# Optimization experiments

Measured on AMD Instinct MI355X. Metric: run time of the kernel, lower is better.

The kernel has to match this reference:

```python
import jax, jax.numpy as jnp
import numpy as np

N_NODES = 100000
N_EDGES = 3200000
D_FEAT = 128
N_LAYERS = 2

def setup_inputs() -> dict:
    key = jax.random.key(0)
    k1, k2, k3, k4 = jax.random.split(key, 4)
    x = jax.random.normal(k1, (N_NODES, D_FEAT), dtype=jnp.float32)
    edge_row = jax.random.randint(k2, (N_EDGES,), 0, N_NODES)  # destination (spmm output row)
    edge_col = jax.random.randint(k3, (N_EDGES,), 0, N_NODES)  # source node
    edge_vals = jax.random.uniform(k4, (N_EDGES,), dtype=jnp.float32)
    scalars = jnp.ones((N_LAYERS,), dtype=jnp.float32)  # per-layer learned scalar (init ones)
    return {"x": x, "edge_row": edge_row, "edge_col": edge_col,
            "edge_vals": edge_vals, "scalars": scalars}

def reference(x, edge_row, edge_col, edge_vals, scalars):
    # ScalarSGC forward with dropout p=0 (identity). Same adjacency each layer.
    for l in range(N_LAYERS):
        h = scalars[l] * x                      # scalar * x
        msg = edge_vals[:, None] * h[edge_col]  # [E, D] gather + scale
        agg = jax.ops.segment_sum(msg, edge_row, num_segments=N_NODES)  # spmm
        x = jax.nn.elu(agg)
    return x
```

## Files before the change

kernel.cpp:

```cpp
#include <hip/hip_runtime.h>
#include <math.h>
#include <stdint.h>


#define D_FEAT 128
#define D2     64
#define SCAN_TILE 1024

#define PB 256
#define PT 1024
#define RB_BITS 9
#define ROWS_PER_BUCKET 512
#define COL_BITS 17
#define CACHE_CAP 17152

__device__ __forceinline__ uint32_t f2bf(float f) {
    uint32_t u = __float_as_uint(f);
    return (u + 0x7FFFu + ((u >> 16) & 1u)) >> 16;
}
__device__ __forceinline__ float bf_lo(uint32_t w) { return __uint_as_float(w << 16); }
__device__ __forceinline__ float bf_hi(uint32_t w) { return __uint_as_float(w & 0xFFFF0000u); }

__global__ void convert_kernel(const float2* __restrict__ xin, uint32_t* __restrict__ xbf, int n2) {
    int i = blockIdx.x * blockDim.x + threadIdx.x;
    if (i < n2) {
        float2 f = xin[i];
        xbf[i] = f2bf(f.x) | (f2bf(f.y) << 16);
    }
}

__global__ __launch_bounds__(PT) void coarse_count_kernel(const int* __restrict__ row,
                                                          int* __restrict__ cnt,
                                                          int E, int nbuck) {
    __shared__ int hist[256];
    const int t = threadIdx.x;
    if (t < 256) hist[t] = 0;
    __syncthreads();
    const int stride = PB * PT;
    for (int i = blockIdx.x * PT + t; i < E; i += stride)
        atomicAdd(&hist[row[i] >> RB_BITS], 1);
    __syncthreads();
    if (t < nbuck) cnt[t * PB + blockIdx.x] = hist[t];
}

__global__ __launch_bounds__(SCAN_TILE) void scan1_kernel(const int* __restrict__ counts,
                                                          int* __restrict__ excl,
                                                          int* __restrict__ tileSums, int n) {
    __shared__ int wsum[16];
    const int tid  = threadIdx.x;
    const int lane = tid & 63;
    const int wave = tid >> 6;
    const int i    = blockIdx.x * SCAN_TILE + tid;

    int v = (i < n) ? counts[i] : 0;
    int incl = v;
    #pragma unroll
    for (int off = 1; off < 64; off <<= 1) {
        int t = __shfl_up(incl, off, 64);
        if (lane >= off) incl += t;
    }
    if (lane == 63) wsum[wave] = incl;
    __syncthreads();
    if (wave == 0) {
        int s = (lane < 16) ? wsum[lane] : 0;
        #pragma unroll
        for (int off = 1; off < 16; off <<= 1) {
            int t = __shfl_up(s, off, 64);
            if (lane >= off) s += t;
        }
        if (lane < 16) wsum[lane] = s;
    }
    __syncthreads();
    int wbase = (wave == 0) ? 0 : wsum[wave - 1];
    if (i < n) excl[i] = wbase + (incl - v);
    if (tid == 0) tileSums[blockIdx.x] = wsum[15];
}

__global__ __launch_bounds__(1024) void scan2_kernel(const int* __restrict__ tileSums,
                                                     int* __restrict__ tileBase,
                                                     int* __restrict__ total_out, int nb) {
    __shared__ int buf[1024];
    const int tid = threadIdx.x;
    int v = (tid < nb) ? tileSums[tid] : 0;
    buf[tid] = v;
    __syncthreads();
    #pragma unroll
    for (int off = 1; off < 1024; off <<= 1) {
        int t = (tid >= off) ? buf[tid - off] : 0;
        __syncthreads();
        buf[tid] += t;
        __syncthreads();
    }
    if (tid < nb) tileBase[tid] = buf[tid] - v;
    if (tid == nb - 1) *total_out = buf[tid];
}

__global__ __launch_bounds__(PT) void partition_kernel(const int* __restrict__ row,
                                                       const int* __restrict__ col,
                                                       const float* __restrict__ val,
                                                       const int* __restrict__ cnt,
                                                       const int* __restrict__ tileBase,
                                                       int2* __restrict__ pack2,
                                                       int E, int nbuck) {
    __shared__ int cur[256];
    const int t = threadIdx.x;
    if (t < nbuck) {
        int idx = t * PB + blockIdx.x;
        cur[t] = cnt[idx] + tileBase[idx >> 10];
    }
    __syncthreads();
    const int stride = PB * PT;
    for (int i = blockIdx.x * PT + t; i < E; i += stride) {
        int r = row[i];
        int pos = atomicAdd(&cur[r >> RB_BITS], 1);
        pack2[pos] = make_int2(col[i] | ((r & (ROWS_PER_BUCKET - 1)) << COL_BITS),
                               __float_as_int(val[i]));
    }
}

__global__ __launch_bounds__(1024) void fine_sort_kernel(const int* __restrict__ cnt,
                                                         const int* __restrict__ tileBase,
                                                         const int2* __restrict__ pack2,
                                                         int2* __restrict__ pack,
                                                         int* __restrict__ offsets,
                                                         int E, int N, int nbuck) {
    extern __shared__ int2 ecache[];
    __shared__ int buf[1024];
    __shared__ int cur[ROWS_PER_BUCKET];
    const int b = blockIdx.x;
    const int t = threadIdx.x;
    const int start = cnt[b << 8] + tileBase[b >> 2];
    const int end   = (b == nbuck - 1) ? E : (cnt[(b + 1) << 8] + tileBase[(b + 1) >> 2]);
    const int n  = end - start;
    const int nc = (n < CACHE_CAP) ? n : CACHE_CAP;

    for (int i = t; i < nc; i += 1024) ecache[i] = pack2[start + i];
    buf[t] = 0;
    __syncthreads();

    for (int i = t; i < n; i += 1024) {
        int key = (i < nc) ? ecache[i].x : pack2[start + i].x;
        atomicAdd(&buf[((unsigned)key) >> COL_BITS], 1);
    }
    __syncthreads();

    int v = buf[t];
    for (int off = 1; off < 1024; off <<= 1) {
        int tv = (t >= off) ? buf[t - off] : 0;
        __syncthreads();
        buf[t] += tv;
        __syncthreads();
    }
    int excl = buf[t] - v;
    if (t < ROWS_PER_BUCKET) {
        int r = (b << RB_BITS) + t;
        if (r < N) offsets[r] = start + excl;
        cur[t] = excl;
    }
    if (b == 0 && t == 0) offsets[N] = E;
    __syncthreads();

    for (int i = t; i < n; i += 1024) {
        int2 w = (i < nc) ? ecache[i] : pack2[start + i];
        int lr = ((unsigned)w.x) >> COL_BITS;
        int p = atomicAdd(&cur[lr], 1);
        pack[start + p] = make_int2(w.x & ((1 << COL_BITS) - 1), w.y);
    }
}

template <int OUT_BF16>
__global__ __launch_bounds__(256) void spmm_elu_kernel(
    const int* __restrict__ offsets, const int2* __restrict__ pack,
    const uint32_t* __restrict__ xin, void* __restrict__ xout,
    const float* __restrict__ scalars, int layer, int N) {
    const int wave = threadIdx.x >> 6;
    const uint32_t lane = threadIdx.x & 63;
    const int r    = blockIdx.x * 4 + wave;
    if (r >= N) return;

    int e = offsets[r];
    const int end = offsets[r + 1];

    float a0x = 0.f, a0y = 0.f, a1x = 0.f, a1y = 0.f;
    float a2x = 0.f, a2y = 0.f, a3x = 0.f, a3y = 0.f;

    for (; e + 4 <= end; e += 4) {
        int2 p0 = pack[e], p1 = pack[e + 1], p2 = pack[e + 2], p3 = pack[e + 3];
        uint32_t w0 = xin[(((uint32_t)p0.x) << 6) + lane];
        uint32_t w1 = xin[(((uint32_t)p1.x) << 6) + lane];
        uint32_t w2 = xin[(((uint32_t)p2.x) << 6) + lane];
        uint32_t w3 = xin[(((uint32_t)p3.x) << 6) + lane];
        float v0 = __int_as_float(p0.y), v1 = __int_as_float(p1.y);
        float v2 = __int_as_float(p2.y), v3 = __int_as_float(p3.y);
        a0x += v0 * bf_lo(w0); a0y += v0 * bf_hi(w0);
        a1x += v1 * bf_lo(w1); a1y += v1 * bf_hi(w1);
        a2x += v2 * bf_lo(w2); a2y += v2 * bf_hi(w2);
        a3x += v3 * bf_lo(w3); a3y += v3 * bf_hi(w3);
    }
    for (; e < end; ++e) {
        int2 p = pack[e];
        uint32_t w = xin[(((uint32_t)p.x) << 6) + lane];
        float v = __int_as_float(p.y);
        a0x += v * bf_lo(w); a0y += v * bf_hi(w);
    }

    float ax = (a0x + a1x) + (a2x + a3x);
    float ay = (a0y + a1y) + (a2y + a3y);
    const float s = scalars[layer];
    ax *= s; ay *= s;
    ax = (ax > 0.f) ? ax : (expf(ax) - 1.f);
    ay = (ay > 0.f) ? ay : (expf(ay) - 1.f);

    if (OUT_BF16) {
        ((uint32_t*)xout)[(size_t)r * D2 + lane] = f2bf(ax) | (f2bf(ay) << 16);
    } else {
        ((float2*)xout)[(size_t)r * D2 + lane] = make_float2(ax, ay);
    }
}

extern "C" void kernel_launch(void* const* d_in, const int* in_sizes, int n_in,
                              void* d_out, int out_size, void* d_ws, size_t ws_size,
                              hipStream_t stream) {
    const float* x         = (const float*)d_in[0];
    const int*   edge_row  = (const int*)d_in[1];
    const int*   edge_col  = (const int*)d_in[2];
    const float* edge_vals = (const float*)d_in[3];
    const float* scalars   = (const float*)d_in[4];

    const int N = in_sizes[0] / D_FEAT;
    const int E = in_sizes[1];
    const int nbuck = (N + ROWS_PER_BUCKET - 1) >> RB_BITS;
    const int M = nbuck * PB;
    const int NB = (M + SCAN_TILE - 1) / SCAN_TILE;

    char*  ws  = (char*)d_ws;
    size_t off = 0;
    auto alloc = [&](size_t bytes) -> void* {
        off = (off + 255) & ~(size_t)255;
        void* p = ws + off;
        off += bytes;
        return p;
    };
    int*      offsets  = (int*)alloc((size_t)(N + 1) * sizeof(int));
    int*      cnt      = (int*)alloc((size_t)(M + 1) * sizeof(int));
    int*      tileSums = (int*)alloc((size_t)NB * sizeof(int));
    int*      tileBase = (int*)alloc((size_t)NB * sizeof(int));
    int2*     pack2    = (int2*)alloc((size_t)E * sizeof(int2));
    int2*     pack     = (int2*)alloc((size_t)E * sizeof(int2));
    uint32_t* xbf      = (uint32_t*)alloc((size_t)N * D2 * sizeof(uint32_t));
    uint32_t* hbf      = (uint32_t*)pack2;
    (void)ws_size;

    convert_kernel<<<(N * D2 + 255) / 256, 256, 0, stream>>>((const float2*)x, xbf, N * D2);
    coarse_count_kernel<<<PB, PT, 0, stream>>>(edge_row, cnt, E, nbuck);
    scan1_kernel<<<NB, SCAN_TILE, 0, stream>>>(cnt, cnt, tileSums, M);
    scan2_kernel<<<1, 1024, 0, stream>>>(tileSums, tileBase, cnt + M, NB);
    partition_kernel<<<PB, PT, 0, stream>>>(edge_row, edge_col, edge_vals, cnt, tileBase,
                                            pack2, E, nbuck);
    fine_sort_kernel<<<nbuck, 1024, (size_t)CACHE_CAP * sizeof(int2), stream>>>(
        cnt, tileBase, pack2, pack, offsets, E, N, nbuck);

    const int nblk = (N + 3) / 4;
    spmm_elu_kernel<1><<<nblk, 256, 0, stream>>>(offsets, pack, xbf, hbf, scalars, 0, N);
    spmm_elu_kernel<0><<<nblk, 256, 0, stream>>>(offsets, pack, hbf, (void*)d_out, scalars, 1, N);
}
```

Before: 435.4 us.

## Split each wave into four edge groups with 16-byte feature loads in SpMM

The SpMM+ELU kernel now has each 16-lane quarter of a wave handle a different edge. Each lane loads a uint4 holding 8 bf16 features, so one wave fetches four neighbour rows at once instead of one 4-byte-per-lane row. Partial sums are combined across the groups with xor shuffles before the scale, ELU and vectorised store. The aim is more memory-level parallelism and fewer loop iterations per row. The cost is extra select logic for picking edges, a padded tail step, and the shuffle reduction.

```diff
diff --git a/kernel.cpp b/kernel.cpp
--- a/kernel.cpp
+++ b/kernel.cpp
@@ -174,47 +174,98 @@
     const uint32_t* __restrict__ xin, void* __restrict__ xout,
     const float* __restrict__ scalars, int layer, int N) {
     const int wave = threadIdx.x >> 6;
-    const uint32_t lane = threadIdx.x & 63;
+    const int lane = threadIdx.x & 63;
+    const int g    = lane >> 4;
+    const int sub  = lane & 15;
     const int r    = blockIdx.x * 4 + wave;
     if (r >= N) return;
 
-    int e = offsets[r];
-    const int end = offsets[r + 1];
-
-    float a0x = 0.f, a0y = 0.f, a1x = 0.f, a1y = 0.f;
-    float a2x = 0.f, a2y = 0.f, a3x = 0.f, a3y = 0.f;
-
+    int e         = __builtin_amdgcn_readfirstlane(offsets[r]);
+    const int end = __builtin_amdgcn_readfirstlane(offsets[r + 1]);
+
+    const uint4* __restrict__ xin4 = (const uint4*)xin;
+
+    float a[8];
+    #pragma unroll
+    for (int k = 0; k < 8; ++k) a[k] = 0.f;
+
+    #define SEL4(PK, CO, VO)                                               \
+        {                                                                  \
+            int2 p0 = (PK)[0], p1 = (PK)[1], p2 = (PK)[2], p3 = (PK)[3];   \
+            int cA = (g & 1) ? p1.x : p0.x, cB = (g & 1) ? p3.x : p2.x;    \
+            int vA = (g & 1) ? p1.y : p0.y, vB = (g & 1) ? p3.y : p2.y;    \
+            CO = (g & 2) ? cB : cA;                                        \
+            VO = __int_as_float((g & 2) ? vB : vA);                        \
+        }
+
+    #define FMA8(W, V)                                                     \
+        a[0] += (V) * bf_lo((W).x); a[1] += (V) * bf_hi((W).x);            \
+        a[2] += (V) * bf_lo((W).y); a[3] += (V) * bf_hi((W).y);            \
+        a[4] += (V) * bf_lo((W).z); a[5] += (V) * bf_hi((W).z);            \
+        a[6] += (V) * bf_lo((W).w); a[7] += (V) * bf_hi((W).w);
+
+    for (; e + 16 <= end; e += 16) {
+        int c0, c1, c2, c3; float v0, v1, v2, v3;
+        SEL4(pack + e,      c0, v0);
+        SEL4(pack + e + 4,  c1, v1);
+        SEL4(pack + e + 8,  c2, v2);
+        SEL4(pack + e + 12, c3, v3);
+        uint4 w0 = xin4[(((uint32_t)c0) << 4) + sub];
+        uint4 w1 = xin4[(((uint32_t)c1) << 4) + sub];
+        uint4 w2 = xin4[(((uint32_t)c2) << 4) + sub];
+        uint4 w3 = xin4[(((uint32_t)c3) << 4) + sub];
+        FMA8(w0, v0); FMA8(w1, v1); FMA8(w2, v2); FMA8(w3, v3);
+    }
     for (; e + 4 <= end; e += 4) {
-        int2 p0 = pack[e], p1 = pack[e + 1], p2 = pack[e + 2], p3 = pack[e + 3];
-        uint32_t w0 = xin[(((uint32_t)p0.x) << 6) + lane];
-        uint32_t w1 = xin[(((uint32_t)p1.x) << 6) + lane];
-        uint32_t w2 = xin[(((uint32_t)p2.x) << 6) + lane];
-        uint32_t w3 = xin[(((uint32_t)p3.x) << 6) + lane];
-        float v0 = __int_as_float(p0.y), v1 = __int_as_float(p1.y);
-        float v2 = __int_as_float(p2.y), v3 = __int_as_float(p3.y);
-        a0x += v0 * bf_lo(w0); a0y += v0 * bf_hi(w0);
-        a1x += v1 * bf_lo(w1); a1y += v1 * bf_hi(w1);
-        a2x += v2 * bf_lo(w2); a2y += v2 * bf_hi(w2);
-        a3x += v3 * bf_lo(w3); a3y += v3 * bf_hi(w3);
-    }
-    for (; e < end; ++e) {
-        int2 p = pack[e];
-        uint32_t w = xin[(((uint32_t)p.x) << 6) + lane];
-        float v = __int_as_float(p.y);
-        a0x += v * bf_lo(w); a0y += v * bf_hi(w);
-    }
-
-    float ax = (a0x + a1x) + (a2x + a3x);
-    float ay = (a0y + a1y) + (a2y + a3y);
+        int c0; float v0;
+        SEL4(pack + e, c0, v0);
+        uint4 w0 = xin4[(((uint32_t)c0) << 4) + sub];
+        FMA8(w0, v0);
+    }
+    if (e < end) {
+        const int rem = end - e;
+        int2 pl = pack[end - 1];
+        int2 p0 = pack[e];
+        int2 p1 = (rem > 1) ? pack[e + 1] : make_int2(pl.x, 0);
+        int2 p2 = (rem > 2) ? pack[e + 2] : make_int2(pl.x, 0);
+        int2 p3 = make_int2(pl.x, 0);
+        int cA = (g & 1) ? p1.x : p0.x, cB = (g & 1) ? p3.x : p2.x;
+        int vA = (g & 1) ? p1.y : p0.y, vB = (g & 1) ? p3.y : p2.y;
+        int c0 = (g & 2) ? cB : cA;
+        float v0 = __int_as_float((g & 2) ? vB : vA);
+        uint4 w0 = xin4[(((uint32_t)c0) << 4) + sub];
+        FMA8(w0, v0);
+    }
+    #undef SEL4
+    #undef FMA8
+
+    #pragma unroll
+    for (int off = 16; off <= 32; off <<= 1) {
+        #pragma unroll
+        for (int k = 0; k < 8; ++k) a[k] += __shfl_xor(a[k], off, 64);
+    }
+
     const float s = scalars[layer];
-    ax *= s; ay *= s;
-    ax = (ax > 0.f) ? ax : (expf(ax) - 1.f);
-    ay = (ay > 0.f) ? ay : (expf(ay) - 1.f);
+    #pragma unroll
+    for (int k = 0; k < 8; ++k) {
+        float x = a[k] * s;
+        a[k] = (x > 0.f) ? x : (expf(x) - 1.f);
+    }
 
     if (OUT_BF16) {
-        ((uint32_t*)xout)[(size_t)r * D2 + lane] = f2bf(ax) | (f2bf(ay) << 16);
+        if (g == 0) {
+            uint4 o;
+            o.x = f2bf(a[0]) | (f2bf(a[1]) << 16);
+            o.y = f2bf(a[2]) | (f2bf(a[3]) << 16);
+            o.z = f2bf(a[4]) | (f2bf(a[5]) << 16);
+            o.w = f2bf(a[6]) | (f2bf(a[7]) << 16);
+            ((uint4*)xout)[(size_t)r * 16 + sub] = o;
+        }
     } else {
-        ((float2*)xout)[(size_t)r * D2 + lane] = make_float2(ax, ay);
+        if (g == 0)
+            ((float4*)xout)[(size_t)r * 32 + sub * 2]     = make_float4(a[0], a[1], a[2], a[3]);
+        else if (g == 1)
+            ((float4*)xout)[(size_t)r * 32 + sub * 2 + 1] = make_float4(a[4], a[5], a[6], a[7]);
     }
 }
 
```

After: 412.8 us. 1.05x faster.
